# Kernel tuning notes

Hardware: AMD Instinct MI355X
Metric: run time of the kernel (lower is better)

The kernel has to match this reference:

```python
import jax, jax.numpy as jnp
import numpy as np

B, IC, OC, OUT_DIM, S = 64, 128, 128, 1024, 2
L = OUT_DIM * S  # 2048


def setup_inputs() -> dict:
    key = jax.random.key(0)
    k1, k2 = jax.random.split(key)
    x = jax.random.normal(k1, (B, IC, L), dtype=jnp.float32)
    weight = jax.random.normal(k2, (OC, IC, L), dtype=jnp.float32)
    return {"x": x, "weight": weight}


def reference(x, weight):
    # Faithful to: (x[:,None]*weight).view(B,OC,IC,-1,2).sum(dims=[-1,-3]) / sqrt(IC)
    # Fused as a single contraction over input_channels and the size-2 patch axis,
    # never materializing the (B,OC,IC,L) intermediate.
    ic = x.shape[1]
    xr = x.reshape(x.shape[0], ic, -1, 2)          # (B, IC, out_dim, 2)
    wr = weight.reshape(weight.shape[0], ic, -1, 2)  # (OC, IC, out_dim, 2)
    out = jnp.einsum('bids,oids->bod', xr, wr)       # (B, OC, out_dim)
    return out / jnp.sqrt(jnp.asarray(ic, dtype=x.dtype))
```

## Files before the change

kernel.cpp:

```cpp
#include <hip/hip_runtime.h>

#define B_SZ   64
#define IC_N   128
#define OC_N   128
#define OUT_D  1024
#define L_N    2048

typedef __attribute__((ext_vector_type(8))) __bf16 bf16x8;
typedef __attribute__((ext_vector_type(4))) float  f32x4;

__device__ __forceinline__ unsigned pack2bf(float lo, float hi) {
    unsigned ul = __builtin_bit_cast(unsigned, lo);
    unsigned uh = __builtin_bit_cast(unsigned, hi);
    ul += 0x7fffu + ((ul >> 16) & 1u);
    uh += 0x7fffu + ((uh >> 16) & 1u);
    return (ul >> 16) | (uh & 0xffff0000u);
}

__global__ __launch_bounds__(512)
void lc1d_fused(const float* __restrict__ x, const float* __restrict__ w,
                float* __restrict__ out) {
    __shared__ __align__(16) unsigned smem[12288];
    unsigned* Xs = smem;
    unsigned* Ws = smem + 4096;

    const int bid = blockIdx.x;
    const int dg  = (bid & 7) * 32 + (bid >> 3);
    const int t = threadIdx.x, wv = t >> 6, lane = t & 63;
    const int col = lane & 15, quad = lane >> 4;

    const int j   = t & 1;
    const int icl = (t >> 1) & 15;
    const int rb  = t >> 5;

    const size_t rowoff  = ((size_t)rb * IC_N + icl) * L_N + (size_t)dg * 8 + 4 * j;
    const float* xp = x + rowoff;
    const float* wp = w + rowoff;
    const size_t RSTRIDE = (size_t)16 * IC_N * L_N;
    const size_t CSTRIDE = (size_t)16 * L_N;

    const int dl = wv & 3, nh = wv >> 2;
    const unsigned* xa = Xs + dl * 1024 + col * 16 + quad * 4;
    const unsigned* wb = Ws + dl * 2048 + (nh * 64 + col) * 16 + quad * 4;

    f32x4 acc[4][4];
#pragma unroll
    for (int mt = 0; mt < 4; ++mt)
#pragma unroll
        for (int nt = 0; nt < 4; ++nt)
            acc[mt][nt] = (f32x4){0.f, 0.f, 0.f, 0.f};

    float4 xv[4], wvv[8];
#pragma unroll
    for (int r = 0; r < 4; ++r) xv[r]  = *(const float4*)(xp + (size_t)r * RSTRIDE);
#pragma unroll
    for (int r = 0; r < 8; ++r) wvv[r] = *(const float4*)(wp + (size_t)r * RSTRIDE);

    for (int c = 0; c < 8; ++c) {
        __syncthreads();

#pragma unroll
        for (int r = 0; r < 4; ++r) {
            const int b_ = rb + 16 * r;
            Xs[(2 * j)     * 1024 + b_ * 16 + icl] = pack2bf(xv[r].x, xv[r].y);
            Xs[(2 * j + 1) * 1024 + b_ * 16 + icl] = pack2bf(xv[r].z, xv[r].w);
        }
#pragma unroll
        for (int r = 0; r < 8; ++r) {
            const int o_ = rb + 16 * r;
            Ws[(2 * j)     * 2048 + o_ * 16 + icl] = pack2bf(wvv[r].x, wvv[r].y);
            Ws[(2 * j + 1) * 2048 + o_ * 16 + icl] = pack2bf(wvv[r].z, wvv[r].w);
        }
        __syncthreads();

        if (c < 7) {
            const float* xq = xp + (size_t)(c + 1) * CSTRIDE;
            const float* wq = wp + (size_t)(c + 1) * CSTRIDE;
#pragma unroll
            for (int r = 0; r < 4; ++r) xv[r]  = *(const float4*)(xq + (size_t)r * RSTRIDE);
#pragma unroll
            for (int r = 0; r < 8; ++r) wvv[r] = *(const float4*)(wq + (size_t)r * RSTRIDE);
        }

        bf16x8 a[4], bfr[4];
#pragma unroll
        for (int mt = 0; mt < 4; ++mt)
            a[mt] = __builtin_bit_cast(bf16x8, *(const uint4*)(xa + mt * 256));
#pragma unroll
        for (int nt = 0; nt < 4; ++nt)
            bfr[nt] = __builtin_bit_cast(bf16x8, *(const uint4*)(wb + nt * 256));
#pragma unroll
        for (int mt = 0; mt < 4; ++mt)
#pragma unroll
            for (int nt = 0; nt < 4; ++nt)
                acc[mt][nt] = __builtin_amdgcn_mfma_f32_16x16x32_bf16(
                    a[mt], bfr[nt], acc[mt][nt], 0, 0, 0);
    }

    const float scale = 0.088388347648318447f;
    float* ep = (float*)smem;
#pragma unroll
    for (int r = 0; r < 4; ++r) {
        __syncthreads();
#pragma unroll
        for (int nt = 0; nt < 4; ++nt)
#pragma unroll
            for (int reg = 0; reg < 4; ++reg) {
                const int b_l = 4 * quad + reg;
                const int o   = nh * 64 + 16 * nt + col;
                ep[(b_l * 128 + o) * 5 + dl] = acc[r][nt][reg] * scale;
            }
        __syncthreads();
#pragma unroll
        for (int pi = 0; pi < 4; ++pi) {
            const int P = t + 512 * pi;
            const int b_l = P >> 7, o = P & 127;
            const float* s = &ep[(size_t)P * 5];
            float4 v;
            v.x = s[0]; v.y = s[1]; v.z = s[2]; v.w = s[3];
            *(float4*)&out[(size_t)((16 * r + b_l) * OC_N + o) * OUT_D + dg * 4] = v;
        }
    }
}

extern "C" void kernel_launch(void* const* d_in, const int* in_sizes, int n_in,
                              void* d_out, int out_size, void* d_ws, size_t ws_size,
                              hipStream_t stream) {
    const float* x = (const float*)d_in[0];
    const float* w = (const float*)d_in[1];
    float* out     = (float*)d_out;
    hipLaunchKernelGGL(lc1d_fused, dim3(256), dim3(512), 0, stream, x, w, out);
}
```

Before: 289.0 us.

## Double-buffer LDS slabs with two-deep register prefetch and per-block chunk stagger

The kernel now keeps two LDS slabs and two register sets of prefetched x/w chunks, so global loads run two chunks ahead and only one barrier is needed per chunk instead of two. Each block also starts its chunk sweep at a different phase (bid & 7), which spreads concurrent memory accesses across address ranges. Launch bounds now request 2 blocks per CU. In exchange, LDS use doubles to 96 KB, which likely still allows only one block per CU, and the extra 48 live prefetch registers plus the tighter register cap raise the risk of spills.

After: 286.1 us. Within noise of the previous version (-1.0%).

```diff
diff --git a/kernel.cpp b/kernel.cpp
--- a/kernel.cpp
+++ b/kernel.cpp
@@ -17,15 +17,14 @@
     return (ul >> 16) | (uh & 0xffff0000u);
 }
 
-__global__ __launch_bounds__(512)
+__global__ __launch_bounds__(512, 2)
 void lc1d_fused(const float* __restrict__ x, const float* __restrict__ w,
                 float* __restrict__ out) {
-    __shared__ __align__(16) unsigned smem[12288];
-    unsigned* Xs = smem;
-    unsigned* Ws = smem + 4096;
+    __shared__ __align__(16) unsigned smem[2][12288];
 
     const int bid = blockIdx.x;
     const int dg  = (bid & 7) * 32 + (bid >> 3);
+    const int phase = bid & 7;
     const int t = threadIdx.x, wv = t >> 6, lane = t & 63;
     const int col = lane & 15, quad = lane >> 4;
 
@@ -39,9 +38,9 @@
     const size_t RSTRIDE = (size_t)16 * IC_N * L_N;
     const size_t CSTRIDE = (size_t)16 * L_N;
 
-    const int dl = wv & 3, nh = wv >> 2;
-    const unsigned* xa = Xs + dl * 1024 + col * 16 + quad * 4;
-    const unsigned* wb = Ws + dl * 2048 + (nh * 64 + col) * 16 + quad * 4;
+    const int dl = wv & 3;
+    const int xoff = dl * 1024 + col * 16 + quad * 4;
+    const int woff = 4096 + dl * 2048 + ((wv >> 2) * 64 + col) * 16 + quad * 4;
 
     f32x4 acc[4][4];
 #pragma unroll
@@ -50,38 +49,37 @@
         for (int nt = 0; nt < 4; ++nt)
             acc[mt][nt] = (f32x4){0.f, 0.f, 0.f, 0.f};
 
-    float4 xv[4], wvv[8];
+    float4 xvA[4], wvA[8], xvB[4], wvB[8];
+
+    auto load_ab = [&](float4* XV, float4* WV, int c) {
+        const float* xq = xp + (size_t)c * CSTRIDE;
+        const float* wq = wp + (size_t)c * CSTRIDE;
 #pragma unroll
-    for (int r = 0; r < 4; ++r) xv[r]  = *(const float4*)(xp + (size_t)r * RSTRIDE);
+        for (int r = 0; r < 4; ++r) XV[r] = *(const float4*)(xq + (size_t)r * RSTRIDE);
 #pragma unroll
-    for (int r = 0; r < 8; ++r) wvv[r] = *(const float4*)(wp + (size_t)r * RSTRIDE);
+        for (int r = 0; r < 8; ++r) WV[r] = *(const float4*)(wq + (size_t)r * RSTRIDE);
+    };
 
-    for (int c = 0; c < 8; ++c) {
-        __syncthreads();
-
+    auto store_slab = [&](int buf, const float4* XV, const float4* WV) {
+        unsigned* Xs = smem[buf];
+        unsigned* Ws = smem[buf] + 4096;
 #pragma unroll
         for (int r = 0; r < 4; ++r) {
             const int b_ = rb + 16 * r;
-            Xs[(2 * j)     * 1024 + b_ * 16 + icl] = pack2bf(xv[r].x, xv[r].y);
-            Xs[(2 * j + 1) * 1024 + b_ * 16 + icl] = pack2bf(xv[r].z, xv[r].w);
+            Xs[(2 * j)     * 1024 + b_ * 16 + icl] = pack2bf(XV[r].x, XV[r].y);
+            Xs[(2 * j + 1) * 1024 + b_ * 16 + icl] = pack2bf(XV[r].z, XV[r].w);
         }
 #pragma unroll
         for (int r = 0; r < 8; ++r) {
             const int o_ = rb + 16 * r;
-            Ws[(2 * j)     * 2048 + o_ * 16 + icl] = pack2bf(wvv[r].x, wvv[r].y);
-            Ws[(2 * j + 1) * 2048 + o_ * 16 + icl] = pack2bf(wvv[r].z, wvv[r].w);
+            Ws[(2 * j)     * 2048 + o_ * 16 + icl] = pack2bf(WV[r].x, WV[r].y);
+            Ws[(2 * j + 1) * 2048 + o_ * 16 + icl] = pack2bf(WV[r].z, WV[r].w);
         }
-        __syncthreads();
+    };
 
-        if (c < 7) {
-            const float* xq = xp + (size_t)(c + 1) * CSTRIDE;
-            const float* wq = wp + (size_t)(c + 1) * CSTRIDE;
-#pragma unroll
-            for (int r = 0; r < 4; ++r) xv[r]  = *(const float4*)(xq + (size_t)r * RSTRIDE);
-#pragma unroll
-            for (int r = 0; r < 8; ++r) wvv[r] = *(const float4*)(wq + (size_t)r * RSTRIDE);
-        }
-
+    auto compute = [&](int buf) {
+        const unsigned* xa = smem[buf] + xoff;
+        const unsigned* wb = smem[buf] + woff;
         bf16x8 a[4], bfr[4];
 #pragma unroll
         for (int mt = 0; mt < 4; ++mt)
@@ -95,10 +93,27 @@
             for (int nt = 0; nt < 4; ++nt)
                 acc[mt][nt] = __builtin_amdgcn_mfma_f32_16x16x32_bf16(
                     a[mt], bfr[nt], acc[mt][nt], 0, 0, 0);
+    };
+
+    load_ab(xvA, wvA, phase);
+    load_ab(xvB, wvB, (phase + 1) & 7);
+
+#pragma unroll
+    for (int cc = 0; cc < 8; cc += 2) {
+        store_slab(0, xvA, wvA);
+        __syncthreads();
+        if (cc + 2 < 8) load_ab(xvA, wvA, (phase + cc + 2) & 7);
+        compute(0);
+
+        store_slab(1, xvB, wvB);
+        __syncthreads();
+        if (cc + 3 < 8) load_ab(xvB, wvB, (phase + cc + 3) & 7);
+        compute(1);
     }
 
     const float scale = 0.088388347648318447f;
     float* ep = (float*)smem;
+    const int nh2 = wv >> 2;
 #pragma unroll
     for (int r = 0; r < 4; ++r) {
         __syncthreads();
@@ -107,7 +122,7 @@
 #pragma unroll
             for (int reg = 0; reg < 4; ++reg) {
                 const int b_l = 4 * quad + reg;
-                const int o   = nh * 64 + 16 * nt + col;
+                const int o   = nh2 * 64 + 16 * nt + col;
                 ep[(b_l * 128 + o) * 5 + dl] = acc[r][nt][reg] * scale;
             }
         __syncthreads();
```

## Split output channels across two blocks and double-buffer LDS slabs

Applied to the files above, without the earlier changes.

The grid doubles to 512 blocks, each covering half the output channels (64) for its d-group, so each block keeps half as many weight registers and accumulators. LDS becomes double-buffered, which removes one barrier per chunk and lets global loads of the next chunk overlap the MFMA work. The chunk order is rotated per XCD to spread memory traffic. In exchange, x is now read twice, once by each channel-half block, and the epilogue staging is adjusted to the 64-channel layout.

After: 315.9 us. +9.3%, slower.

```diff
diff --git a/kernel.cpp b/kernel.cpp
--- a/kernel.cpp
+++ b/kernel.cpp
@@ -17,15 +17,18 @@
     return (ul >> 16) | (uh & 0xffff0000u);
 }
 
-__global__ __launch_bounds__(512)
+__global__ __launch_bounds__(512, 4)
 void lc1d_fused(const float* __restrict__ x, const float* __restrict__ w,
                 float* __restrict__ out) {
-    __shared__ __align__(16) unsigned smem[12288];
-    unsigned* Xs = smem;
-    unsigned* Ws = smem + 4096;
+    __shared__ __align__(16) unsigned smem[2][8192];
 
     const int bid = blockIdx.x;
-    const int dg  = (bid & 7) * 32 + (bid >> 3);
+    const int xcd = bid & 7;
+    const int g   = bid >> 3;
+    const int dg  = xcd * 32 + (g & 31);
+    const int och = g >> 5;
+    const int o0  = och * 64;
+
     const int t = threadIdx.x, wv = t >> 6, lane = t & 63;
     const int col = lane & 15, quad = lane >> 4;
 
@@ -33,68 +36,76 @@
     const int icl = (t >> 1) & 15;
     const int rb  = t >> 5;
 
-    const size_t rowoff  = ((size_t)rb * IC_N + icl) * L_N + (size_t)dg * 8 + 4 * j;
-    const float* xp = x + rowoff;
-    const float* wp = w + rowoff;
-    const size_t RSTRIDE = (size_t)16 * IC_N * L_N;
-    const size_t CSTRIDE = (size_t)16 * L_N;
+    const float* xp = x + ((size_t)rb * IC_N + icl) * L_N + (size_t)dg * 8 + 4 * j;
+    const float* wp = w + ((size_t)(o0 + rb) * IC_N + icl) * L_N + (size_t)dg * 8 + 4 * j;
+    const size_t RS = (size_t)16 * IC_N * L_N;
+    const size_t CS = (size_t)16 * L_N;
 
-    const int dl = wv & 3, nh = wv >> 2;
-    const unsigned* xa = Xs + dl * 1024 + col * 16 + quad * 4;
-    const unsigned* wb = Ws + dl * 2048 + (nh * 64 + col) * 16 + quad * 4;
+    const int dl = wv & 3, bh = wv >> 2;
+    const int xread = dl * 1024 + (bh * 32 + col) * 16 + quad * 4;
+    const int wread = 4096 + dl * 1024 + col * 16 + quad * 4;
 
-    f32x4 acc[4][4];
+    f32x4 acc[2][4];
 #pragma unroll
-    for (int mt = 0; mt < 4; ++mt)
+    for (int mt = 0; mt < 2; ++mt)
 #pragma unroll
         for (int nt = 0; nt < 4; ++nt)
             acc[mt][nt] = (f32x4){0.f, 0.f, 0.f, 0.f};
 
-    float4 xv[4], wvv[8];
+    float4 xv[4], wvv[4];
+
+    auto load_chunk = [&](int c) {
+        const int cc = (c + xcd) & 7;
+        const float* xq = xp + (size_t)cc * CS;
+        const float* wq = wp + (size_t)cc * CS;
 #pragma unroll
-    for (int r = 0; r < 4; ++r) xv[r]  = *(const float4*)(xp + (size_t)r * RSTRIDE);
+        for (int r = 0; r < 4; ++r) xv[r]  = *(const float4*)(xq + (size_t)r * RS);
 #pragma unroll
-    for (int r = 0; r < 8; ++r) wvv[r] = *(const float4*)(wp + (size_t)r * RSTRIDE);
+        for (int r = 0; r < 4; ++r) wvv[r] = *(const float4*)(wq + (size_t)r * RS);
+    };
 
-    for (int c = 0; c < 8; ++c) {
-        __syncthreads();
-
+    auto store_slab = [&](int buf) {
+        unsigned* Xs = smem[buf];
+        unsigned* Ws = smem[buf] + 4096;
 #pragma unroll
         for (int r = 0; r < 4; ++r) {
-            const int b_ = rb + 16 * r;
-            Xs[(2 * j)     * 1024 + b_ * 16 + icl] = pack2bf(xv[r].x, xv[r].y);
-            Xs[(2 * j + 1) * 1024 + b_ * 16 + icl] = pack2bf(xv[r].z, xv[r].w);
+            const int row = (rb + 16 * r) * 16 + icl;
+            Xs[(2 * j) * 1024 + row]     = pack2bf(xv[r].x, xv[r].y);
+            Xs[(2 * j + 1) * 1024 + row] = pack2bf(xv[r].z, xv[r].w);
         }
 #pragma unroll
-        for (int r = 0; r < 8; ++r) {
-            const int o_ = rb + 16 * r;
-            Ws[(2 * j)     * 2048 + o_ * 16 + icl] = pack2bf(wvv[r].x, wvv[r].y);
-            Ws[(2 * j + 1) * 2048 + o_ * 16 + icl] = pack2bf(wvv[r].z, wvv[r].w);
+        for (int r = 0; r < 4; ++r) {
+            const int row = (rb + 16 * r) * 16 + icl;
+            Ws[(2 * j) * 1024 + row]     = pack2bf(wvv[r].x, wvv[r].y);
+            Ws[(2 * j + 1) * 1024 + row] = pack2bf(wvv[r].z, wvv[r].w);
         }
-        __syncthreads();
+    };
 
-        if (c < 7) {
-            const float* xq = xp + (size_t)(c + 1) * CSTRIDE;
-            const float* wq = wp + (size_t)(c + 1) * CSTRIDE;
+    auto compute = [&](int buf) {
+        const unsigned* base = smem[buf];
+        bf16x8 a[2], b[4];
 #pragma unroll
-            for (int r = 0; r < 4; ++r) xv[r]  = *(const float4*)(xq + (size_t)r * RSTRIDE);
-#pragma unroll
-            for (int r = 0; r < 8; ++r) wvv[r] = *(const float4*)(wq + (size_t)r * RSTRIDE);
-        }
-
-        bf16x8 a[4], bfr[4];
-#pragma unroll
-        for (int mt = 0; mt < 4; ++mt)
-            a[mt] = __builtin_bit_cast(bf16x8, *(const uint4*)(xa + mt * 256));
+        for (int mt = 0; mt < 2; ++mt)
+            a[mt] = __builtin_bit_cast(bf16x8, *(const uint4*)(base + xread + mt * 256));
 #pragma unroll
         for (int nt = 0; nt < 4; ++nt)
-            bfr[nt] = __builtin_bit_cast(bf16x8, *(const uint4*)(wb + nt * 256));
+            b[nt] = __builtin_bit_cast(bf16x8, *(const uint4*)(base + wread + nt * 256));
 #pragma unroll
-        for (int mt = 0; mt < 4; ++mt)
+        for (int mt = 0; mt < 2; ++mt)
 #pragma unroll
             for (int nt = 0; nt < 4; ++nt)
                 acc[mt][nt] = __builtin_amdgcn_mfma_f32_16x16x32_bf16(
-                    a[mt], bfr[nt], acc[mt][nt], 0, 0, 0);
+                    a[mt], b[nt], acc[mt][nt], 0, 0, 0);
+    };
+
+    load_chunk(0);
+#pragma unroll
+    for (int c = 0; c < 8; ++c) {
+        const int buf = c & 1;
+        store_slab(buf);
+        __syncthreads();
+        if (c < 7) load_chunk(c + 1);
+        compute(buf);
     }
 
     const float scale = 0.088388347648318447f;
@@ -102,23 +113,26 @@
 #pragma unroll
     for (int r = 0; r < 4; ++r) {
         __syncthreads();
+        if (bh == (r >> 1)) {
+            const int mt = r & 1;
 #pragma unroll
-        for (int nt = 0; nt < 4; ++nt)
+            for (int nt = 0; nt < 4; ++nt)
 #pragma unroll
-            for (int reg = 0; reg < 4; ++reg) {
-                const int b_l = 4 * quad + reg;
-                const int o   = nh * 64 + 16 * nt + col;
-                ep[(b_l * 128 + o) * 5 + dl] = acc[r][nt][reg] * scale;
-            }
+                for (int reg = 0; reg < 4; ++reg) {
+                    const int b_l = 4 * quad + reg;
+                    const int o   = 16 * nt + col;
+                    ep[(b_l * 64 + o) * 5 + dl] = acc[mt][nt][reg] * scale;
+                }
+        }
         __syncthreads();
 #pragma unroll
-        for (int pi = 0; pi < 4; ++pi) {
+        for (int pi = 0; pi < 2; ++pi) {
             const int P = t + 512 * pi;
-            const int b_l = P >> 7, o = P & 127;
+            const int b_l = P >> 6, o = P & 63;
             const float* s = &ep[(size_t)P * 5];
             float4 v;
             v.x = s[0]; v.y = s[1]; v.z = s[2]; v.w = s[3];
-            *(float4*)&out[(size_t)((16 * r + b_l) * OC_N + o) * OUT_D + dg * 4] = v;
+            *(float4*)&out[(size_t)((16 * r + b_l) * OC_N + o0 + o) * OUT_D + dg * 4] = v;
         }
     }
 }
@@ -129,5 +143,5 @@
     const float* x = (const float*)d_in[0];
     const float* w = (const float*)d_in[1];
     float* out     = (float*)d_out;
-    hipLaunchKernelGGL(lc1d_fused, dim3(256), dim3(512), 0, stream, x, w, out);
+    hipLaunchKernelGGL(lc1d_fused, dim3(512), dim3(512), 0, stream, x, w, out);
 }
```
